# Kernel optimization log

Measured on AMD Instinct MI355X. Metric: run time of the kernel, lower is better.

The kernel has to match this reference:

```python
import jax, jax.numpy as jnp
import numpy as np

B, C, H, W, K = 64, 64, 32, 32, 1024  # C == dim_dict, K == size_dict
BETA = 0.25


def setup_inputs() -> dict:
    key = jax.random.key(0)
    k1, k2, k3 = jax.random.split(key, 3)
    return {
        "z_from_encoder": jax.random.normal(k1, (B, C, H, W), dtype=jnp.float32),
        "codebook": jax.random.normal(k2, (K, C), dtype=jnp.float32),
        "codebook_weight": jax.random.normal(k3, (K,), dtype=jnp.float32),
        "flg_train": 1,
    }


def reference(z_from_encoder, codebook, codebook_weight, flg_train):
    # NCHW -> NHWC, flatten to (N, D)
    z = jnp.transpose(z_from_encoder, (0, 2, 3, 1))
    zf = z.reshape(-1, z.shape[-1])                      # (N, D)
    # squared euclidean distances via expansion (N, K)
    d = (jnp.sum(zf ** 2, axis=1, keepdims=True)
         + jnp.sum(codebook ** 2, axis=1)
         - 2.0 * zf @ codebook.T)
    idx = jnp.argmin(d, axis=1)                          # (N,)
    # one-hot @ codebook == gather
    z_q = codebook[idx].reshape(z.shape)                 # (B, H, W, D)
    if flg_train:
        loss = (BETA * jnp.mean((jax.lax.stop_gradient(z_q) - z) ** 2)
                + jnp.mean((z_q - jax.lax.stop_gradient(z)) ** 2))
    else:
        loss = jnp.float32(0.0)
    # straight-through estimator
    z_q_st = z + jax.lax.stop_gradient(z_q - z)
    # codebook usage histogram -> perplexity
    n_tok = zf.shape[0]
    e_mean = jnp.zeros((codebook.shape[0],), z.dtype).at[idx].add(1.0) / n_tok
    perplexity = jnp.exp(-jnp.sum(e_mean * jnp.log(e_mean + 1e-10)))
    z_q_out = jnp.transpose(z_q_st, (0, 3, 1, 2))        # back to NCHW
    return z_q_out, loss, perplexity
```

## Files before the change

### kernel.cpp

```cpp
#include <hip/hip_runtime.h>


typedef __attribute__((ext_vector_type(8))) short short8;
typedef __attribute__((ext_vector_type(4))) float float4v;

#define KK     1024
#define DD     64
#define NTOK   65536
#define NELEM  4194304
#define MTILE  128
#define NBLK   (NTOK / MTILE)

#define WS_CBF   0
#define WS_C2H   262144
#define WS_HIST  266240
#define WS_LOSS  270336

__device__ __forceinline__ unsigned bf16_rne(float x) {
    unsigned u = __float_as_uint(x);
    return (u + 0x7fffu + ((u >> 16) & 1u)) >> 16;
}

__global__ __launch_bounds__(256) void prep_kernel(
    const float* __restrict__ cb, ushort* __restrict__ cbf,
    float* __restrict__ c2h, int* __restrict__ hist, float* __restrict__ loss_part) {
    int tid = threadIdx.x;
    int gid = blockIdx.x * 256 + tid;
    if (gid < KK) hist[gid] = 0;
    if (gid < 64) loss_part[gid] = 0.f;

    int n  = gid >> 4;
    int dg = (gid & 15) * 4;
    const float* cp = cb + n * DD + dg;
    float4v v = *(const float4v*)cp;
    float s = v.x * v.x + v.y * v.y + v.z * v.z + v.w * v.w;
    s += __shfl_xor(s, 1); s += __shfl_xor(s, 2);
    s += __shfl_xor(s, 4); s += __shfl_xor(s, 8);
    if ((gid & 15) == 0) c2h[n] = -0.5f * s;

    int c = n >> 4, col = n & 15;
#pragma unroll
    for (int jj = 0; jj < 4; jj++) {
        int d = dg + jj;
        float x = ((const float*)cp)[jj];
        unsigned hb = bf16_rne(x);
        float hf = __uint_as_float(hb << 16);
        unsigned lb = bf16_rne(x - hf);
        int st = d >> 5, kq = (d & 31) >> 3, j = d & 7;
        int lane = kq * 16 + col;
        cbf[((c * 4 + 0 * 2 + st) * 64 + lane) * 8 + j] = (ushort)hb;
        cbf[((c * 4 + 1 * 2 + st) * 64 + lane) * 8 + j] = (ushort)lb;
    }
}

__global__ __launch_bounds__(256, 4) void vq_kernel(
    const float* __restrict__ z, const float* __restrict__ cb,
    const ushort* __restrict__ cbf, const float* __restrict__ c2h,
    float* __restrict__ out, float* __restrict__ loss_part, int* __restrict__ hist) {
    __shared__ int   s_idx[MTILE];
    __shared__ float s_q[MTILE * 65];
    __shared__ float s_red[4];

    int tid  = threadIdx.x;
    int lane = tid & 63, wave = tid >> 6;
    int quad = lane >> 4, col = lane & 15;
    int tokbase = blockIdx.x * MTILE;
    int b = tokbase >> 10, hwb = tokbase & 1023;
    const float* zb = z + b * 65536 + hwb;

    short8 ah[2][2], al[2][2];
#pragma unroll
    for (int g = 0; g < 2; g++) {
        int rel = wave * 32 + g * 16 + col;
#pragma unroll
        for (int st = 0; st < 2; st++) {
            short8 h8, l8;
#pragma unroll
            for (int j = 0; j < 8; j++) {
                int d = st * 32 + quad * 8 + j;
                float x = zb[d * 1024 + rel];
                unsigned hb = bf16_rne(x);
                float hf = __uint_as_float(hb << 16);
                unsigned lb = bf16_rne(x - hf);
                h8[j] = (short)hb; l8[j] = (short)lb;
            }
            ah[g][st] = h8; al[g][st] = l8;
        }
    }

    float best[2][4]; int bidx[2][4];
#pragma unroll
    for (int g = 0; g < 2; g++)
#pragma unroll
        for (int r = 0; r < 4; r++) { best[g][r] = -1e38f; bidx[g][r] = 0; }

    for (int c = 0; c < 64; c++) {
        float ini = c2h[c * 16 + col];
        const ushort* cp = cbf + c * 2048;
        short8 bh0 = *(const short8*)(cp + (0 * 64 + lane) * 8);
        short8 bh1 = *(const short8*)(cp + (1 * 64 + lane) * 8);
        short8 bl0 = *(const short8*)(cp + (2 * 64 + lane) * 8);
        short8 bl1 = *(const short8*)(cp + (3 * 64 + lane) * 8);
        int code = c * 16 + col;
#pragma unroll
        for (int g = 0; g < 2; g++) {
            float4v a0 = {ini, ini, ini, ini};
            float4v a1 = {0.f, 0.f, 0.f, 0.f};
            a0 = __builtin_amdgcn_mfma_f32_16x16x32_bf16(ah[g][0], bh0, a0, 0, 0, 0);
            a1 = __builtin_amdgcn_mfma_f32_16x16x32_bf16(ah[g][1], bh1, a1, 0, 0, 0);
            a0 = __builtin_amdgcn_mfma_f32_16x16x32_bf16(ah[g][0], bl0, a0, 0, 0, 0);
            a1 = __builtin_amdgcn_mfma_f32_16x16x32_bf16(ah[g][1], bl1, a1, 0, 0, 0);
            a0 = __builtin_amdgcn_mfma_f32_16x16x32_bf16(al[g][0], bh0, a0, 0, 0, 0);
            a1 = __builtin_amdgcn_mfma_f32_16x16x32_bf16(al[g][1], bh1, a1, 0, 0, 0);
            a0 = __builtin_amdgcn_mfma_f32_16x16x32_bf16(al[g][0], bl0, a0, 0, 0, 0);
            a1 = __builtin_amdgcn_mfma_f32_16x16x32_bf16(al[g][1], bl1, a1, 0, 0, 0);
#pragma unroll
            for (int r = 0; r < 4; r++) {
                float s = a0[r] + a1[r];
                if (s > best[g][r]) { best[g][r] = s; bidx[g][r] = code; }
            }
        }
    }

#pragma unroll
    for (int g = 0; g < 2; g++) {
#pragma unroll
        for (int r = 0; r < 4; r++) {
            float s = best[g][r]; int ix = bidx[g][r];
#pragma unroll
            for (int m = 1; m <= 8; m <<= 1) {
                float so = __shfl_xor(s, m);
                int   io = __shfl_xor(ix, m);
                if (so > s || (so == s && io < ix)) { s = so; ix = io; }
            }
            if (col == 0) {
                int t = wave * 32 + g * 16 + quad * 4 + r;
                s_idx[t] = ix;
                atomicAdd(&hist[ix], 1);
            }
        }
    }
    __syncthreads();

#pragma unroll
    for (int p = 0; p < 32; p++) {
        int i = p * 256 + tid;
        int t = i >> 6, d = i & 63;
        s_q[t * 65 + d] = cb[s_idx[t] * 64 + d];
    }
    __syncthreads();

    float ls = 0.f;
#pragma unroll 4
    for (int p = 0; p < 32; p++) {
        int i = p * 256 + tid;
        int d = i >> 7, t = i & 127;
        int a = d * 1024 + t;
        float zv = zb[a];
        float q  = s_q[t * 65 + d];
        float df = q - zv;
        out[b * 65536 + hwb + a] = zv + df;
        ls = fmaf(df, df, ls);
    }
#pragma unroll
    for (int off = 32; off; off >>= 1) ls += __shfl_down(ls, off);
    if (lane == 0) s_red[wave] = ls;
    __syncthreads();
    if (tid == 0) {
        float v = (s_red[0] + s_red[1]) + (s_red[2] + s_red[3]);
        atomicAdd(&loss_part[blockIdx.x & 63], v);
    }
}

__global__ __launch_bounds__(1024) void finalize_kernel(
    const int* __restrict__ hist, const float* __restrict__ loss_part,
    const int* __restrict__ flg, float* __restrict__ out) {
    __shared__ float red[16];
    int   k = threadIdx.x;
    float e = (float)hist[k] * (1.0f / 65536.0f);
    float v = e * logf(e + 1e-10f);
#pragma unroll
    for (int off = 32; off; off >>= 1) v += __shfl_down(v, off);
    if ((k & 63) == 0) red[k >> 6] = v;
    __syncthreads();
    if (k == 0) {
        float s = 0.f;
#pragma unroll
        for (int i = 0; i < 16; i++) s += red[i];
        out[NELEM + 1] = expf(-s);

        float ls = 0.f;
        for (int i = 0; i < 64; i++) ls += loss_part[i];
        float m    = ls * (1.0f / (float)NELEM);
        out[NELEM] = (*flg) ? (0.25f * m + m) : 0.0f;
    }
}

extern "C" void kernel_launch(void* const* d_in, const int* in_sizes, int n_in,
                              void* d_out, int out_size, void* d_ws, size_t ws_size,
                              hipStream_t stream) {
    const float* z   = (const float*)d_in[0];
    const float* cb  = (const float*)d_in[1];
    const int*   flg = (const int*)d_in[3];

    float* out = (float*)d_out;
    char*  ws  = (char*)d_ws;

    ushort* cbf       = (ushort*)(ws + WS_CBF);
    float*  c2h       = (float*)(ws + WS_C2H);
    int*    hist      = (int*)(ws + WS_HIST);
    float*  loss_part = (float*)(ws + WS_LOSS);

    prep_kernel<<<64, 256, 0, stream>>>(cb, cbf, c2h, hist, loss_part);
    vq_kernel<<<NBLK, 256, 0, stream>>>(z, cb, cbf, c2h, out, loss_part, hist);
    finalize_kernel<<<1, 1024, 0, stream>>>(hist, loss_part, flg, out);
}
```

Before: 145.5 us.

## Split codebook search across waves, halve token tile, prefetch codebook fragments

New measurement: 122.4 us. 15.8% less time.

```diff
diff --git a/kernel.cpp b/kernel.cpp
--- a/kernel.cpp
+++ b/kernel.cpp
@@ -4,12 +4,7 @@
 typedef __attribute__((ext_vector_type(8))) short short8;
 typedef __attribute__((ext_vector_type(4))) float float4v;
 
-#define KK     1024
-#define DD     64
-#define NTOK   65536
-#define NELEM  4194304
-#define MTILE  128
-#define NBLK   (NTOK / MTILE)
+#define NELEM 4194304
 
 #define WS_CBF   0
 #define WS_C2H   262144
@@ -24,54 +19,70 @@
 __global__ __launch_bounds__(256) void prep_kernel(
     const float* __restrict__ cb, ushort* __restrict__ cbf,
     float* __restrict__ c2h, int* __restrict__ hist, float* __restrict__ loss_part) {
-    int tid = threadIdx.x;
-    int gid = blockIdx.x * 256 + tid;
-    if (gid < KK) hist[gid] = 0;
-    if (gid < 64) loss_part[gid] = 0.f;
-
-    int n  = gid >> 4;
-    int dg = (gid & 15) * 4;
-    const float* cp = cb + n * DD + dg;
-    float4v v = *(const float4v*)cp;
-    float s = v.x * v.x + v.y * v.y + v.z * v.z + v.w * v.w;
-    s += __shfl_xor(s, 1); s += __shfl_xor(s, 2);
-    s += __shfl_xor(s, 4); s += __shfl_xor(s, 8);
-    if ((gid & 15) == 0) c2h[n] = -0.5f * s;
-
-    int c = n >> 4, col = n & 15;
-#pragma unroll
-    for (int jj = 0; jj < 4; jj++) {
-        int d = dg + jj;
-        float x = ((const float*)cp)[jj];
+    __shared__ float s_c2[2][16];
+    int tid  = threadIdx.x;
+    int lane = tid & 63, wave = tid >> 6;
+    int quad = lane >> 4, col = lane & 15;
+    int bx   = blockIdx.x;
+
+    if (bx >= 64) {
+        hist[(bx - 64) * 256 + tid] = 0;
+        if (bx == 64 && tid < 64) loss_part[tid] = 0.f;
+        return;
+    }
+    int c = bx, fid = wave;
+    int st = fid & 1, split = fid >> 1;
+    int code  = c * 16 + col;
+    int dbase = st * 32 + quad * 8;
+    const float* cp = cb + code * 64 + dbase;
+    float4v v0 = *(const float4v*)cp;
+    float4v v1 = *(const float4v*)(cp + 4);
+    float xs[8] = {v0.x, v0.y, v0.z, v0.w, v1.x, v1.y, v1.z, v1.w};
+    short8 frag;
+    float ssq = 0.f;
+#pragma unroll
+    for (int j = 0; j < 8; j++) {
+        float x = xs[j];
+        ssq = fmaf(x, x, ssq);
         unsigned hb = bf16_rne(x);
-        float hf = __uint_as_float(hb << 16);
-        unsigned lb = bf16_rne(x - hf);
-        int st = d >> 5, kq = (d & 31) >> 3, j = d & 7;
-        int lane = kq * 16 + col;
-        cbf[((c * 4 + 0 * 2 + st) * 64 + lane) * 8 + j] = (ushort)hb;
-        cbf[((c * 4 + 1 * 2 + st) * 64 + lane) * 8 + j] = (ushort)lb;
-    }
+        if (split == 0) frag[j] = (short)hb;
+        else            frag[j] = (short)bf16_rne(x - __uint_as_float(hb << 16));
+    }
+    *(short8*)(cbf + ((c * 4 + fid) * 64 + lane) * 8) = frag;
+    if (split == 0) {
+        ssq += __shfl_xor(ssq, 16);
+        ssq += __shfl_xor(ssq, 32);
+        if (quad == 0) s_c2[st][col] = ssq;
+    }
+    __syncthreads();
+    if (tid < 16) c2h[c * 16 + tid] = -0.5f * (s_c2[0][tid] + s_c2[1][tid]);
 }
 
 __global__ __launch_bounds__(256, 4) void vq_kernel(
     const float* __restrict__ z, const float* __restrict__ cb,
     const ushort* __restrict__ cbf, const float* __restrict__ c2h,
-    float* __restrict__ out, float* __restrict__ loss_part, int* __restrict__ hist) {
-    __shared__ int   s_idx[MTILE];
-    __shared__ float s_q[MTILE * 65];
+    float* __restrict__ out, float* __restrict__ loss_part, int* __restrict__ hist)
+{
+    __shared__ float s_q[64 * 65];
+    __shared__ float s_ms[2][64];
+    __shared__ int   s_mi[2][64];
+    __shared__ int   s_idx[64];
     __shared__ float s_red[4];
 
     int tid  = threadIdx.x;
     int lane = tid & 63, wave = tid >> 6;
     int quad = lane >> 4, col = lane & 15;
-    int tokbase = blockIdx.x * MTILE;
-    int b = tokbase >> 10, hwb = tokbase & 1023;
-    const float* zb = z + b * 65536 + hwb;
+    int bx   = blockIdx.x;
+
+    int tokbase = bx * 64;
+    int bb = tokbase >> 10, hwb = tokbase & 1023;
+    const float* zb = z + bb * 65536 + hwb;
+    int tokhalf = wave & 1, khalf = wave >> 1;
 
     short8 ah[2][2], al[2][2];
 #pragma unroll
     for (int g = 0; g < 2; g++) {
-        int rel = wave * 32 + g * 16 + col;
+        int rel = tokhalf * 32 + g * 16 + col;
 #pragma unroll
         for (int st = 0; st < 2; st++) {
             short8 h8, l8;
@@ -80,9 +91,8 @@
                 int d = st * 32 + quad * 8 + j;
                 float x = zb[d * 1024 + rel];
                 unsigned hb = bf16_rne(x);
-                float hf = __uint_as_float(hb << 16);
-                unsigned lb = bf16_rne(x - hf);
-                h8[j] = (short)hb; l8[j] = (short)lb;
+                h8[j] = (short)hb;
+                l8[j] = (short)bf16_rne(x - __uint_as_float(hb << 16));
             }
             ah[g][st] = h8; al[g][st] = l8;
         }
@@ -94,30 +104,44 @@
 #pragma unroll
         for (int r = 0; r < 4; r++) { best[g][r] = -1e38f; bidx[g][r] = 0; }
 
-    for (int c = 0; c < 64; c++) {
-        float ini = c2h[c * 16 + col];
-        const ushort* cp = cbf + c * 2048;
-        short8 bh0 = *(const short8*)(cp + (0 * 64 + lane) * 8);
-        short8 bh1 = *(const short8*)(cp + (1 * 64 + lane) * 8);
-        short8 bl0 = *(const short8*)(cp + (2 * 64 + lane) * 8);
-        short8 bl1 = *(const short8*)(cp + (3 * 64 + lane) * 8);
-        int code = c * 16 + col;
-#pragma unroll
-        for (int g = 0; g < 2; g++) {
-            float4v a0 = {ini, ini, ini, ini};
-            float4v a1 = {0.f, 0.f, 0.f, 0.f};
-            a0 = __builtin_amdgcn_mfma_f32_16x16x32_bf16(ah[g][0], bh0, a0, 0, 0, 0);
-            a1 = __builtin_amdgcn_mfma_f32_16x16x32_bf16(ah[g][1], bh1, a1, 0, 0, 0);
-            a0 = __builtin_amdgcn_mfma_f32_16x16x32_bf16(ah[g][0], bl0, a0, 0, 0, 0);
-            a1 = __builtin_amdgcn_mfma_f32_16x16x32_bf16(ah[g][1], bl1, a1, 0, 0, 0);
-            a0 = __builtin_amdgcn_mfma_f32_16x16x32_bf16(al[g][0], bh0, a0, 0, 0, 0);
-            a1 = __builtin_amdgcn_mfma_f32_16x16x32_bf16(al[g][1], bh1, a1, 0, 0, 0);
-            a0 = __builtin_amdgcn_mfma_f32_16x16x32_bf16(al[g][0], bl0, a0, 0, 0, 0);
-            a1 = __builtin_amdgcn_mfma_f32_16x16x32_bf16(al[g][1], bl1, a1, 0, 0, 0);
-#pragma unroll
-            for (int r = 0; r < 4; r++) {
-                float s = a0[r] + a1[r];
-                if (s > best[g][r]) { best[g][r] = s; bidx[g][r] = code; }
+    int cbase = khalf * 32;
+    const ushort* cw = cbf + lane * 8;
+    {
+        const ushort* p0 = cw + cbase * 2048;
+        short8 nb0 = *(const short8*)(p0 + 0);
+        short8 nb1 = *(const short8*)(p0 + 512);
+        short8 nb2 = *(const short8*)(p0 + 1024);
+        short8 nb3 = *(const short8*)(p0 + 1536);
+        float  nini = c2h[cbase * 16 + col];
+        for (int cc = 0; cc < 32; cc++) {
+            short8 bh0 = nb0, bh1 = nb1, bl0 = nb2, bl1 = nb3;
+            float  ini = nini;
+            if (cc < 31) {
+                const ushort* np = cw + (cbase + cc + 1) * 2048;
+                nb0 = *(const short8*)(np + 0);
+                nb1 = *(const short8*)(np + 512);
+                nb2 = *(const short8*)(np + 1024);
+                nb3 = *(const short8*)(np + 1536);
+                nini = c2h[(cbase + cc + 1) * 16 + col];
+            }
+            int code = (cbase + cc) * 16 + col;
+#pragma unroll
+            for (int g = 0; g < 2; g++) {
+                float4v a0 = {ini, ini, ini, ini};
+                float4v a1 = {0.f, 0.f, 0.f, 0.f};
+                a0 = __builtin_amdgcn_mfma_f32_16x16x32_bf16(ah[g][0], bh0, a0, 0, 0, 0);
+                a1 = __builtin_amdgcn_mfma_f32_16x16x32_bf16(ah[g][1], bh1, a1, 0, 0, 0);
+                a0 = __builtin_amdgcn_mfma_f32_16x16x32_bf16(ah[g][0], bl0, a0, 0, 0, 0);
+                a1 = __builtin_amdgcn_mfma_f32_16x16x32_bf16(ah[g][1], bl1, a1, 0, 0, 0);
+                a0 = __builtin_amdgcn_mfma_f32_16x16x32_bf16(al[g][0], bh0, a0, 0, 0, 0);
+                a1 = __builtin_amdgcn_mfma_f32_16x16x32_bf16(al[g][1], bh1, a1, 0, 0, 0);
+                a0 = __builtin_amdgcn_mfma_f32_16x16x32_bf16(al[g][0], bl0, a0, 0, 0, 0);
+                a1 = __builtin_amdgcn_mfma_f32_16x16x32_bf16(al[g][1], bl1, a1, 0, 0, 0);
+#pragma unroll
+                for (int r = 0; r < 4; r++) {
+                    float s = a0[r] + a1[r];
+                    if (s > best[g][r]) { best[g][r] = s; bidx[g][r] = code; }
+                }
             }
         }
     }
@@ -134,16 +158,24 @@
                 if (so > s || (so == s && io < ix)) { s = so; ix = io; }
             }
             if (col == 0) {
-                int t = wave * 32 + g * 16 + quad * 4 + r;
-                s_idx[t] = ix;
-                atomicAdd(&hist[ix], 1);
+                int t = tokhalf * 32 + g * 16 + quad * 4 + r;
+                s_ms[khalf][t] = s; s_mi[khalf][t] = ix;
             }
         }
     }
     __syncthreads();
 
-#pragma unroll
-    for (int p = 0; p < 32; p++) {
+    if (tid < 64) {
+        float s0 = s_ms[0][tid], s1 = s_ms[1][tid];
+        int   i0 = s_mi[0][tid], i1 = s_mi[1][tid];
+        int   ix = (s1 > s0) ? i1 : i0;
+        s_idx[tid] = ix;
+        atomicAdd(&hist[ix], 1);
+    }
+    __syncthreads();
+
+#pragma unroll
+    for (int p = 0; p < 16; p++) {
         int i = p * 256 + tid;
         int t = i >> 6, d = i & 63;
         s_q[t * 65 + d] = cb[s_idx[t] * 64 + d];
@@ -152,14 +184,14 @@
 
     float ls = 0.f;
 #pragma unroll 4
-    for (int p = 0; p < 32; p++) {
+    for (int p = 0; p < 16; p++) {
         int i = p * 256 + tid;
-        int d = i >> 7, t = i & 127;
+        int d = i >> 6, t = i & 63;
         int a = d * 1024 + t;
         float zv = zb[a];
         float q  = s_q[t * 65 + d];
         float df = q - zv;
-        out[b * 65536 + hwb + a] = zv + df;
+        out[bb * 65536 + hwb + a] = zv + df;
         ls = fmaf(df, df, ls);
     }
 #pragma unroll
@@ -168,7 +200,7 @@
     __syncthreads();
     if (tid == 0) {
         float v = (s_red[0] + s_red[1]) + (s_red[2] + s_red[3]);
-        atomicAdd(&loss_part[blockIdx.x & 63], v);
+        atomicAdd(&loss_part[bx & 63], v);
     }
 }
 
@@ -211,7 +243,7 @@
     int*    hist      = (int*)(ws + WS_HIST);
     float*  loss_part = (float*)(ws + WS_LOSS);
 
-    prep_kernel<<<64, 256, 0, stream>>>(cb, cbf, c2h, hist, loss_part);
-    vq_kernel<<<NBLK, 256, 0, stream>>>(z, cb, cbf, c2h, out, loss_part, hist);
+    prep_kernel<<<68, 256, 0, stream>>>(cb, cbf, c2h, hist, loss_part);
+    vq_kernel<<<1024, 256, 0, stream>>>(z, cb, cbf, c2h, out, loss_part, hist);
     finalize_kernel<<<1, 1024, 0, stream>>>(hist, loss_part, flg, out);
 }
```
